# Kernel optimization log

Measured on AMD Instinct MI355X. Metric: run time of the kernel, lower is better.

The kernel has to match this reference:

```python
import jax, jax.numpy as jnp
import numpy as np
from jax import lax


def _conv(x, w, b):
    # NCHW x OIHW, stride 1, VALID padding (matches nn.Conv2d padding=0)
    y = lax.conv_general_dilated(x, w, (1, 1), 'VALID',
                                 dimension_numbers=('NCHW', 'OIHW', 'NCHW'))
    return y + b[None, :, None, None]


def _maxpool2(x):
    return lax.reduce_window(x, -jnp.inf, lax.max, (1, 1, 2, 2), (1, 1, 2, 2), 'VALID')


def setup_inputs() -> dict:
    key = jax.random.key(0)
    ks = jax.random.split(key, 8)
    B, C, H, W = 4096, 3, 32, 32
    E, NC = 8, 1000  # out_dim (=n learners), num_classes
    inp = {
        'x': jax.random.normal(ks[0], (B, C, H, W), jnp.float32),
        'conv1_w': jax.random.normal(ks[1], (1, 3, 5, 5), jnp.float32) * 0.1,
        'conv1_b': jnp.zeros((1,), jnp.float32),
        'conv2_w': jax.random.normal(ks[2], (2, 1, 5, 5), jnp.float32) * 0.1,
        'conv2_b': jnp.zeros((2,), jnp.float32),
        'conv3_w': jax.random.normal(ks[3], (4, 2, 5, 5), jnp.float32) * 0.1,
        'conv3_b': jnp.zeros((4,), jnp.float32),
        'fc_w': jax.random.normal(ks[4], (E, 4), jnp.float32) * 0.5,
        'fc_b': jnp.zeros((E,), jnp.float32),
        'ens_w': jax.random.normal(ks[5], (E, C * H * W, NC), jnp.float32) * 0.02,
        'ens_b': jnp.zeros((E, NC), jnp.float32),
        'k': 2,
    }
    return inp


def reference(x, conv1_w, conv1_b, conv2_w, conv2_b, conv3_w, conv3_b,
              fc_w, fc_b, ens_w, ens_b, k):
    B = x.shape[0]
    # --- selector CNN stem ---
    h = jax.nn.relu(_conv(x, conv1_w, conv1_b))   # [B,1,28,28]
    h = _maxpool2(h)                              # [B,1,14,14]
    h = jax.nn.relu(_conv(h, conv2_w, conv2_b))   # [B,2,10,10]
    h = _maxpool2(h)                              # [B,2,5,5]
    h = jax.nn.relu(_conv(h, conv3_w, conv3_b))   # [B,4,1,1]
    h = h.reshape(B, -1)                          # [B,4]
    z = h @ fc_w.T + fc_b                         # [B,E]
    # L2NormalizationLayer with clamp(min=1e-9)
    z = z / jnp.clip(jnp.linalg.norm(z, axis=-1, keepdims=True), 1e-9, None)
    # TopK -> one-hot routing mask (straight-through style forward)
    _, idx = lax.top_k(z, k)                      # [B,k]
    mask = jax.nn.one_hot(idx, z.shape[-1], dtype=z.dtype).sum(-2)  # [B,E] in {0,1}
    # --- frozen ensemble: linear weak learners, combined via mask ---
    xf = x.reshape(B, -1)                          # [B,F]
    outs = jnp.einsum('bf,efc->bec', xf, ens_w) + ens_b[None]  # [B,E,NC]
    return (outs * mask[:, :, None]).sum(axis=1)   # [B,NC]
```

## Files before the change

kernel.cpp:

```cpp
#include <hip/hip_runtime.h>
#include <hip/hip_bf16.h>
#include <stdint.h>

#define B_SZ 4096
#define F_SZ 3072
#define NCLS 1000
#define NE 8
#define NPAD 1024
#define CAP 4096
#define KSPLIT 2
#define KCH (F_SZ / KSPLIT)

#define OFF_CNT   0
#define OFF_LIST  1024
#define OFF_PAIR  132096
#define OFF_XB    262144
#define OFF_WT    25427968

typedef unsigned short u16;
typedef __attribute__((ext_vector_type(8))) short short8v;
typedef __attribute__((ext_vector_type(4))) float f32x4;

__device__ __forceinline__ u16 f2bf(float f) {
  unsigned int u = __float_as_uint(f);
  u = (u + 0x7FFFu + ((u >> 16) & 1u)) >> 16;
  return (u16)u;
}

__device__ __forceinline__ void gll16(const void* g, void* l) {
  __builtin_amdgcn_global_load_lds(
      (const __attribute__((address_space(1))) void*)g,
      (__attribute__((address_space(3))) void*)l, 16, 0, 0);
}

__global__ __launch_bounds__(256) void transpose_w(const float* __restrict__ ensw,
                                                   u16* __restrict__ wt) {
  __shared__ u16 tile[64 * 264];
  int t = threadIdx.x;
  int n0 = blockIdx.x * 64, k0 = blockIdx.y * 256, e = blockIdx.z;
  const float* src = ensw + (size_t)e * (F_SZ * NCLS);
  int kr = t >> 4, nq = (t & 15) * 4;
  for (int it = 0; it < 16; ++it) {
    int kk = it * 16 + kr;
    const float* sp = src + (size_t)(k0 + kk) * NCLS + n0 + nq;
    int n = n0 + nq;
    float4 v = make_float4(0.f, 0.f, 0.f, 0.f);
    if (n + 3 < NCLS) v = *(const float4*)sp;
    else {
      if (n     < NCLS) v.x = sp[0];
      if (n + 1 < NCLS) v.y = sp[1];
      if (n + 2 < NCLS) v.z = sp[2];
      if (n + 3 < NCLS) v.w = sp[3];
    }
    u16* d = tile + nq * 264 + kk;
    d[0]   = f2bf(v.x);
    d[264] = f2bf(v.y);
    d[528] = f2bf(v.z);
    d[792] = f2bf(v.w);
  }
  __syncthreads();
  int kc = t & 31, nr = t >> 5;
  for (int it = 0; it < 8; ++it) {
    int n = it * 8 + nr;
    uint4 pk = *(const uint4*)(tile + n * 264 + kc * 8);
    *(uint4*)(wt + ((size_t)(e * NPAD + n0 + n)) * F_SZ + k0 + kc * 8) = pk;
  }
}

#define XST 36
#define XCH 1152
__global__ __launch_bounds__(128) void selector(
    const float* __restrict__ x,
    const float* __restrict__ w1, const float* __restrict__ b1,
    const float* __restrict__ w2, const float* __restrict__ b2,
    const float* __restrict__ w3, const float* __restrict__ b3,
    const float* __restrict__ fw, const float* __restrict__ fb,
    u16* __restrict__ xb16, int* __restrict__ cnt, int* __restrict__ list,
    int* __restrict__ expair) {
  __shared__ float wgt[384];
  __shared__ float S[2][4704];
  int t = threadIdx.x;
  for (int i = t; i < 372; i += 128) {
    float v;
    if      (i <  75) v = w1[i];
    else if (i <  76) v = b1[i - 75];
    else if (i < 126) v = w2[i - 76];
    else if (i < 128) v = b2[i - 126];
    else if (i < 328) v = w3[i - 128];
    else if (i < 332) v = b3[i - 328];
    else if (i < 364) v = fw[i - 332];
    else              v = fb[i - 364];
    wgt[i] = v;
  }
  int w = t >> 6, l = t & 63;
  int b = blockIdx.x * 2 + w;
  float* xs   = S[w];
  float* buf1 = xs + 3456;
  float* p1   = xs + 4240;
  float* buf2 = xs + 4436;
  float* p2   = xs + 4636;
  float* hb   = xs + 4686;
  float* zb   = xs + 4690;

  const float4* gx = (const float4*)(x + (size_t)b * F_SZ);
  ushort4* gxb = (ushort4*)(xb16 + (size_t)b * F_SZ);
  for (int it = 0; it < 12; ++it) {
    int idx = it * 64 + l;
    float4 v = gx[idx];
    int f = idx * 4;
    int c = f >> 10, rem = f & 1023, y = rem >> 5, xc = rem & 31;
    *(float4*)(xs + c * XCH + y * XST + xc) = v;
    ushort4 h4;
    h4.x = f2bf(v.x); h4.y = f2bf(v.y); h4.z = f2bf(v.z); h4.w = f2bf(v.w);
    gxb[idx] = h4;
  }
  __syncthreads();

  if (l < 56) {
    int y = l >> 1, xh = l & 1;
    float acc[14];
#pragma unroll
    for (int xc = 0; xc < 14; ++xc) acc[xc] = wgt[75];
    for (int c = 0; c < 3; ++c)
      for (int i = 0; i < 5; ++i) {
        const float4* rb = (const float4*)(xs + c * XCH + (y + i) * XST) + xh * 3;
        float a[20];
#pragma unroll
        for (int q = 0; q < 5; ++q) {
          float4 v = rb[q];
          a[q * 4] = v.x; a[q * 4 + 1] = v.y; a[q * 4 + 2] = v.z; a[q * 4 + 3] = v.w;
        }
        if (xh) {
#pragma unroll
          for (int q = 0; q < 18; ++q) a[q] = a[q + 2];
        }
        const float* wp = wgt + c * 25 + i * 5;
        float W0 = wp[0], W1 = wp[1], W2 = wp[2], W3 = wp[3], W4 = wp[4];
#pragma unroll
        for (int xc = 0; xc < 14; ++xc)
          acc[xc] += a[xc] * W0 + a[xc + 1] * W1 + a[xc + 2] * W2 + a[xc + 3] * W3 + a[xc + 4] * W4;
      }
#pragma unroll
    for (int xc = 0; xc < 14; ++xc) buf1[y * 28 + xh * 14 + xc] = fmaxf(acc[xc], 0.f);
  }
  __syncthreads();

  for (int it = 0; it < 4; ++it) {
    int p = it * 64 + l;
    if (p < 196) {
      int py = p / 14, px = p % 14;
      const float* r0 = buf1 + (2 * py) * 28 + 2 * px;
      p1[p] = fmaxf(fmaxf(r0[0], r0[1]), fmaxf(r0[28], r0[29]));
    }
  }
  __syncthreads();

  for (int it = 0; it < 4; ++it) {
    int p = it * 64 + l;
    if (p < 200) {
      int o = p / 100, rem = p % 100, yy = rem / 10, xx = rem % 10;
      float acc = wgt[126 + o];
      const float* wp = wgt + 76 + o * 25;
#pragma unroll
      for (int i = 0; i < 5; ++i)
#pragma unroll
        for (int j = 0; j < 5; ++j) acc += p1[(yy + i) * 14 + xx + j] * wp[i * 5 + j];
      buf2[p] = fmaxf(acc, 0.f);
    }
  }
  __syncthreads();

  if (l < 50) {
    int o = l / 25, rem = l % 25, yy = rem / 5, xx = rem % 5;
    const float* r0 = buf2 + o * 100 + (2 * yy) * 10 + 2 * xx;
    p2[l] = fmaxf(fmaxf(r0[0], r0[1]), fmaxf(r0[10], r0[11]));
  }
  __syncthreads();

  if (l < 4) {
    float acc = wgt[328 + l];
    const float* wp = wgt + 128 + l * 50;
#pragma unroll
    for (int cc = 0; cc < 50; ++cc) acc += p2[cc] * wp[cc];
    hb[l] = fmaxf(acc, 0.f);
  }
  __syncthreads();

  if (l < 8) {
    float acc = wgt[364 + l];
    const float* wp = wgt + 332 + l * 4;
#pragma unroll
    for (int j = 0; j < 4; ++j) acc += hb[j] * wp[j];
    zb[l] = acc;
  }
  __syncthreads();

  if (l == 0) {
    float zz[8];
#pragma unroll
    for (int e = 0; e < 8; ++e) zz[e] = zb[e];
    int e1 = 0; float v1 = zz[0];
    for (int e = 1; e < 8; ++e) if (zz[e] > v1) { v1 = zz[e]; e1 = e; }
    int e2 = -1; float v2 = 0.f;
    for (int e = 0; e < 8; ++e) {
      if (e == e1) continue;
      if (e2 < 0 || zz[e] > v2) { v2 = zz[e]; e2 = e; }
    }
    int p1i = atomicAdd(&cnt[e1], 1); list[e1 * CAP + p1i] = b;
    int p2i = atomicAdd(&cnt[e2], 1); list[e2 * CAP + p2i] = b;
    expair[b] = e1 | (e2 << 8);
  }
}

__global__ __launch_bounds__(256) void bias_init(const int* __restrict__ expair,
                                                 const float* __restrict__ ensb,
                                                 float* __restrict__ out) {
  int b = blockIdx.x;
  int t = threadIdx.x;
  if (t >= 250) return;
  int pr = expair[b];
  const float4* p1 = (const float4*)(ensb + (size_t)(pr & 255) * NCLS);
  const float4* p2 = (const float4*)(ensb + (size_t)((pr >> 8) & 255) * NCLS);
  float4* op = (float4*)(out + (size_t)b * NCLS);
  float4 a = p1[t], c = p2[t];
  float4 r; r.x = a.x + c.x; r.y = a.y + c.y; r.z = a.z + c.z; r.w = a.w + c.w;
  op[t] = r;
}

__global__ __launch_bounds__(256, 4) void moe_gemm(const u16* __restrict__ xb,
                                                   const u16* __restrict__ wt,
                                                   const int* __restrict__ cnt,
                                                   const int* __restrict__ list,
                                                   float* __restrict__ out) {
  __shared__ u16 As[8192];
  __shared__ u16 Bs[8192];
  __shared__ int idx_s[128];
  int e = blockIdx.z >> 1, ks = blockIdx.z & 1;
  int cnt_e = cnt[e];
  int m0 = blockIdx.y * 128;
  if (m0 >= cnt_e) return;
  int n0 = blockIdx.x * 128;
  int t = threadIdx.x;
  const int* lst = list + e * CAP;
  if (t < 128) idx_s[t] = lst[min(m0 + t, cnt_e - 1)];
  __syncthreads();

  int tr = t >> 3, ts = t & 7;
  int g  = ts ^ (tr & 7);
  const u16* pA[4]; const u16* pB[4]; int ldst[4];
#pragma unroll
  for (int q = 0; q < 4; ++q) {
    int row = q * 32 + tr;
    pA[q] = xb + (size_t)idx_s[row] * F_SZ + ks * KCH + g * 8;
    pB[q] = wt + ((size_t)(e * NPAD + n0 + row)) * F_SZ + ks * KCH + g * 8;
    ldst[q] = (q * 256 + t) * 8;
  }

  int w = t >> 6, l = t & 63;
  int lr = l & 15, hk = l >> 4;
  int wrow = (w >> 1) * 64, wcol = (w & 1) * 64;
  int rA[4], rB[4];
#pragma unroll
  for (int i = 0; i < 4; ++i) {
    rA[i] = (wrow + i * 16 + lr) * 64;
    rB[i] = (wcol + i * 16 + lr) * 64;
  }
  int sw0 = ((hk    ) ^ (lr & 7)) * 8;
  int sw1 = ((hk + 4) ^ (lr & 7)) * 8;

#pragma unroll
  for (int q = 0; q < 4; ++q) { gll16(pA[q], &As[ldst[q]]); pA[q] += 64; }
#pragma unroll
  for (int q = 0; q < 4; ++q) { gll16(pB[q], &Bs[ldst[q]]); pB[q] += 64; }

  f32x4 acc[4][4] = {};
  for (int s = 0; s < KCH / 64; ++s) {
    __syncthreads();
    short8v av[2][4], bv[2][4];
#pragma unroll
    for (int i = 0; i < 4; ++i) {
      av[0][i] = *(const short8v*)(&As[rA[i] + sw0]);
      av[1][i] = *(const short8v*)(&As[rA[i] + sw1]);
      bv[0][i] = *(const short8v*)(&Bs[rB[i] + sw0]);
      bv[1][i] = *(const short8v*)(&Bs[rB[i] + sw1]);
    }
#pragma unroll
    for (int h = 0; h < 2; ++h)
#pragma unroll
      for (int i = 0; i < 4; ++i)
#pragma unroll
        for (int j = 0; j < 4; ++j)
          acc[i][j] = __builtin_amdgcn_mfma_f32_16x16x32_bf16(av[h][i], bv[h][j], acc[i][j], 0, 0, 0);
    if (s < KCH / 64 - 1) {
      __syncthreads();
#pragma unroll
      for (int q = 0; q < 4; ++q) { gll16(pA[q], &As[ldst[q]]); pA[q] += 64; }
#pragma unroll
      for (int q = 0; q < 4; ++q) { gll16(pB[q], &Bs[ldst[q]]); pB[q] += 64; }
    }
  }

#pragma unroll
  for (int i = 0; i < 4; ++i) {
#pragma unroll
    for (int r = 0; r < 4; ++r) {
      int mt = wrow + i * 16 + hk * 4 + r;
      if (m0 + mt < cnt_e) {
        float* orow = out + (size_t)idx_s[mt] * NCLS;
#pragma unroll
        for (int j = 0; j < 4; ++j) {
          int col = n0 + wcol + j * 16 + lr;
          if (col < NCLS) unsafeAtomicAdd(orow + col, acc[i][j][r]);
        }
      }
    }
  }
}

extern "C" void kernel_launch(void* const* d_in, const int* in_sizes, int n_in,
                              void* d_out, int out_size, void* d_ws, size_t ws_size,
                              hipStream_t stream) {
  const float* x   = (const float*)d_in[0];
  const float* w1  = (const float*)d_in[1];
  const float* b1  = (const float*)d_in[2];
  const float* w2  = (const float*)d_in[3];
  const float* b2  = (const float*)d_in[4];
  const float* w3  = (const float*)d_in[5];
  const float* b3  = (const float*)d_in[6];
  const float* fw  = (const float*)d_in[7];
  const float* fb  = (const float*)d_in[8];
  const float* ensw = (const float*)d_in[9];
  const float* ensb = (const float*)d_in[10];
  float* out = (float*)d_out;

  uint8_t* ws = (uint8_t*)d_ws;
  int* cnt    = (int*)(ws + OFF_CNT);
  int* list   = (int*)(ws + OFF_LIST);
  int* expair = (int*)(ws + OFF_PAIR);
  u16* xb16   = (u16*)(ws + OFF_XB);
  u16* wt     = (u16*)(ws + OFF_WT);

  hipMemsetAsync(cnt, 0, 64, stream);
  transpose_w<<<dim3(16, 12, 8), 256, 0, stream>>>(ensw, wt);
  selector<<<2048, 128, 0, stream>>>(x, w1, b1, w2, b2, w3, b3, fw, fb,
                                     xb16, cnt, list, expair);
  bias_init<<<4096, 256, 0, stream>>>(expair, ensb, out);
  moe_gemm<<<dim3(8, 32, 16), 256, 0, stream>>>(xb16, wt, cnt, list, out);
}
```

Before: 439.6 us.

## Double-buffer MoE GEMM LDS with K=32 stages and 1D expert-interleaved grid

The MoE GEMM now keeps two LDS buffers and issues the next K-slice's global-to-LDS loads before computing on the current one, so loads overlap MFMA work and each iteration needs one barrier instead of two. The K step shrinks from 64 to 32 to keep total LDS the same, and the swizzle changes to match. The grid becomes 1D with expert/ksplit in the low bits, so concurrently scheduled blocks are spread across experts and early-exiting empty tiles are interleaved. The cost is twice as many loop iterations with less MFMA work per barrier.

```diff
diff --git a/kernel.cpp b/kernel.cpp
--- a/kernel.cpp
+++ b/kernel.cpp
@@ -232,72 +232,67 @@
                                                    const int* __restrict__ cnt,
                                                    const int* __restrict__ list,
                                                    float* __restrict__ out) {
-  __shared__ u16 As[8192];
-  __shared__ u16 Bs[8192];
+  __shared__ u16 As[2][4096];
+  __shared__ u16 Bs[2][4096];
   __shared__ int idx_s[128];
-  int e = blockIdx.z >> 1, ks = blockIdx.z & 1;
+  int id = blockIdx.x;
+  int gq = id & 15, q = id >> 4;
+  int e  = gq >> 1, ks = gq & 1;
   int cnt_e = cnt[e];
-  int m0 = blockIdx.y * 128;
+  int m0 = (q >> 3) * 128;
   if (m0 >= cnt_e) return;
-  int n0 = blockIdx.x * 128;
+  int n0 = (q & 7) * 128;
   int t = threadIdx.x;
   const int* lst = list + e * CAP;
   if (t < 128) idx_s[t] = lst[min(m0 + t, cnt_e - 1)];
   __syncthreads();
 
-  int tr = t >> 3, ts = t & 7;
-  int g  = ts ^ (tr & 7);
-  const u16* pA[4]; const u16* pB[4]; int ldst[4];
-#pragma unroll
-  for (int q = 0; q < 4; ++q) {
-    int row = q * 32 + tr;
-    pA[q] = xb + (size_t)idx_s[row] * F_SZ + ks * KCH + g * 8;
-    pB[q] = wt + ((size_t)(e * NPAD + n0 + row)) * F_SZ + ks * KCH + g * 8;
-    ldst[q] = (q * 256 + t) * 8;
-  }
+  int r0 = t >> 2, sl = t & 3;
+  int gch = sl ^ (r0 & 3);
+  size_t kbase = (size_t)ks * KCH + gch * 8;
+  const u16* pA0 = xb + (size_t)idx_s[r0]      * F_SZ + kbase;
+  const u16* pA1 = xb + (size_t)idx_s[r0 + 64] * F_SZ + kbase;
+  const u16* pB0 = wt + ((size_t)(e * NPAD + n0 + r0))      * F_SZ + kbase;
+  const u16* pB1 = wt + ((size_t)(e * NPAD + n0 + r0 + 64)) * F_SZ + kbase;
+  int d0 = t * 8, d1 = (256 + t) * 8;
 
   int w = t >> 6, l = t & 63;
   int lr = l & 15, hk = l >> 4;
   int wrow = (w >> 1) * 64, wcol = (w & 1) * 64;
+  int swz = (hk ^ (lr & 3)) * 8;
   int rA[4], rB[4];
 #pragma unroll
   for (int i = 0; i < 4; ++i) {
-    rA[i] = (wrow + i * 16 + lr) * 64;
-    rB[i] = (wcol + i * 16 + lr) * 64;
-  }
-  int sw0 = ((hk    ) ^ (lr & 7)) * 8;
-  int sw1 = ((hk + 4) ^ (lr & 7)) * 8;
-
-#pragma unroll
-  for (int q = 0; q < 4; ++q) { gll16(pA[q], &As[ldst[q]]); pA[q] += 64; }
-#pragma unroll
-  for (int q = 0; q < 4; ++q) { gll16(pB[q], &Bs[ldst[q]]); pB[q] += 64; }
+    rA[i] = (wrow + i * 16 + lr) * 32 + swz;
+    rB[i] = (wcol + i * 16 + lr) * 32 + swz;
+  }
+
+  gll16(pA0, &As[0][d0]); gll16(pA1, &As[0][d1]);
+  gll16(pB0, &Bs[0][d0]); gll16(pB1, &Bs[0][d1]);
+  pA0 += 32; pA1 += 32; pB0 += 32; pB1 += 32;
+  __syncthreads();
 
   f32x4 acc[4][4] = {};
-  for (int s = 0; s < KCH / 64; ++s) {
+  const int NS = KCH / 32;
+  for (int s = 0; s < NS; ++s) {
+    int cur = s & 1;
+    if (s + 1 < NS) {
+      int nxt = cur ^ 1;
+      gll16(pA0, &As[nxt][d0]); gll16(pA1, &As[nxt][d1]);
+      gll16(pB0, &Bs[nxt][d0]); gll16(pB1, &Bs[nxt][d1]);
+      pA0 += 32; pA1 += 32; pB0 += 32; pB1 += 32;
+    }
+    short8v av[4], bv[4];
+#pragma unroll
+    for (int i = 0; i < 4; ++i) av[i] = *(const short8v*)(&As[cur][rA[i]]);
+#pragma unroll
+    for (int j = 0; j < 4; ++j) bv[j] = *(const short8v*)(&Bs[cur][rB[j]]);
+#pragma unroll
+    for (int i = 0; i < 4; ++i)
+#pragma unroll
+      for (int j = 0; j < 4; ++j)
+        acc[i][j] = __builtin_amdgcn_mfma_f32_16x16x32_bf16(av[i], bv[j], acc[i][j], 0, 0, 0);
     __syncthreads();
-    short8v av[2][4], bv[2][4];
-#pragma unroll
-    for (int i = 0; i < 4; ++i) {
-      av[0][i] = *(const short8v*)(&As[rA[i] + sw0]);
-      av[1][i] = *(const short8v*)(&As[rA[i] + sw1]);
-      bv[0][i] = *(const short8v*)(&Bs[rB[i] + sw0]);
-      bv[1][i] = *(const short8v*)(&Bs[rB[i] + sw1]);
-    }
-#pragma unroll
-    for (int h = 0; h < 2; ++h)
-#pragma unroll
-      for (int i = 0; i < 4; ++i)
-#pragma unroll
-        for (int j = 0; j < 4; ++j)
-          acc[i][j] = __builtin_amdgcn_mfma_f32_16x16x32_bf16(av[h][i], bv[h][j], acc[i][j], 0, 0, 0);
-    if (s < KCH / 64 - 1) {
-      __syncthreads();
-#pragma unroll
-      for (int q = 0; q < 4; ++q) { gll16(pA[q], &As[ldst[q]]); pA[q] += 64; }
-#pragma unroll
-      for (int q = 0; q < 4; ++q) { gll16(pB[q], &Bs[ldst[q]]); pB[q] += 64; }
-    }
   }
 
 #pragma unroll
@@ -345,5 +340,5 @@
   selector<<<2048, 128, 0, stream>>>(x, w1, b1, w2, b2, w3, b3, fw, fb,
                                      xb16, cnt, list, expair);
   bias_init<<<4096, 256, 0, stream>>>(expair, ensb, out);
-  moe_gemm<<<dim3(8, 32, 16), 256, 0, stream>>>(xb16, wt, cnt, list, out);
-}
+  moe_gemm<<<4096, 256, 0, stream>>>(xb16, wt, cnt, list, out);
+}
```

Result: slower. 577.4 us (+31.4%).
